# Kernel optimization log

Hardware: AMD Instinct MI355X
Metric: run time of the kernel (lower is better)

## Reference

```python
import jax, jax.numpy as jnp
import numpy as np

N, H, W, C, CK, ITER = 4, 256, 256, 8, 2, 4
HID = 2 * C
C2 = C * C


def project(x, w1, b1, w2, b2, w3, b3):
    # flax Project: Dense->gelu->Dense->gelu->Dense (gelu approximate=tanh, jax default)
    h = jax.nn.gelu(x @ w1 + b1)
    h = jax.nn.gelu(h @ w2 + b2)
    return h @ w3 + b3


def setup_inputs() -> dict:
    key = jax.random.key(0)
    ks = jax.random.split(key, 40)
    d = {}
    d['u'] = jax.random.normal(ks[0], (N, H, W, C), jnp.float32)
    d['k'] = jax.random.normal(ks[1], (N, H, W, CK), jnp.float32)
    idx = 2
    # gamma MLP (in CK), delta MLP (in CK), greens real/imag MLPs (in 2)
    for nm, fin in zip(['g', 'dl', 'fr', 'fi'], [CK, CK, 2, 2]):
        for li, (fi_, fo) in enumerate([(fin, HID), (HID, HID), (HID, C2)]):
            d[f'{nm}_w{li+1}'] = jax.random.normal(ks[idx], (fi_, fo), jnp.float32) / np.sqrt(fi_).astype(np.float32)
            d[f'{nm}_b{li+1}'] = jnp.zeros((fo,), jnp.float32)
            idx += 1
    d['bias'] = jax.random.normal(ks[idx], (C,), jnp.float32)
    return d


def reference(u, k, g_w1, g_b1, g_w2, g_b2, g_w3, g_b3,
              dl_w1, dl_b1, dl_w2, dl_b2, dl_w3, dl_b3,
              fr_w1, fr_b1, fr_w2, fr_b2, fr_w3, fr_b3,
              fi_w1, fi_b1, fi_w2, fi_b2, fi_w3, fi_b3, bias):
    # per-pixel gamma / delta matrices: (N,H,W,C,C), scaled by 1/C^2 as in original
    gmat = (project(k, g_w1, g_b1, g_w2, g_b2, g_w3, g_b3) / C2).reshape(N, H, W, C, C)
    dmat = (project(k, dl_w1, dl_b1, dl_w2, dl_b2, dl_w3, dl_b3) / C2).reshape(N, H, W, C, C)
    # spectral Green's filter on the rfft grid; meshgrid(kx, ky) -> (W, H//2+1)
    kx = jnp.fft.rfftfreq(H, d=1.0 / H)
    ky = jnp.fft.fftfreq(W, d=1.0 / W)
    Kx, Ky = jnp.meshgrid(kx, ky)
    K = jnp.stack([Kx, Ky], axis=-1).astype(jnp.float32)  # (W, H//2+1, 2)
    filt_r = project(K, fr_w1, fr_b1, fr_w2, fr_b2, fr_w3, fr_b3)
    filt_i = project(K, fi_w1, fi_b1, fi_w2, fi_b2, fi_w3, fi_b3)
    filt = ((filt_r + 1j * filt_i) / C2).reshape(W, H // 2 + 1, C, C)  # H==W
    for _ in range(ITER):
        local = 2.0 * u - jnp.einsum('nhwj,nhwjk->nhwk', u, gmat)
        du = jnp.einsum('nhwj,nhwjk->nhwk', u, dmat)
        uf = jnp.fft.rfftn(du, axes=(1, 2))  # (N,H,W//2+1,C) complex
        gu = jnp.fft.irfftn(jnp.einsum('nhwj,hwjk->nhwk', uf, filt), axes=(1, 2))
        u = local + jnp.einsum('nhwj,nhwjk->nhwk', gu, gmat)
    return jax.nn.gelu(u + bias)
```

## Files before the change

kernel.cpp:

```cpp
#include <hip/hip_runtime.h>
#include <math.h>

#define NB 4
#define HB 256
#define WB 256
#define CB 8
#define NPIX (NB*HB*WB)
#define W2B 129
#define TWO_PI_F 6.283185307179586f

typedef float f32x4 __attribute__((ext_vector_type(4)));

__device__ __forceinline__ float gelu_f(float x){
    float z = 0.7978845608028654f*(x + 0.044715f*x*x*x);
    return x * __builtin_amdgcn_rcpf(1.0f + __expf(-2.0f*z));
}

__device__ __forceinline__ unsigned pack_bf16x2(float a, float b){
    unsigned ua = __float_as_uint(a), ub = __float_as_uint(b);
    ua = (ua + 0x7FFFu + ((ua >> 16) & 1u)) >> 16;
    ub = (ub + 0x7FFFu + ((ub >> 16) & 1u)) >> 16;
    return ua | (ub << 16);
}
__device__ __forceinline__ float2 unpack_bf16x2(unsigned v){
    return make_float2(__uint_as_float(v << 16), __uint_as_float(v & 0xFFFF0000u));
}

__device__ __forceinline__ void ldcp(float* dst, const float* __restrict__ src, int n, int t){
    for (int i = t; i < n; i += 256) dst[i] = src[i];
}

__global__ __launch_bounds__(256) void prep_kernel(
    const float* __restrict__ kin,
    const float* gw1,const float* gb1,const float* gw2,const float* gb2,const float* gw3,const float* gb3,
    const float* dw1,const float* db1,const float* dw2,const float* db2,const float* dw3,const float* db3,
    const float* fw1,const float* fb1,const float* fw2,const float* fb2,const float* fw3,const float* fb3,
    const float* iw1,const float* ib1,const float* iw2,const float* ib2,const float* iw3,const float* ib3,
    unsigned* __restrict__ gmat, unsigned* __restrict__ dmat,
    unsigned* __restrict__ fpack)
{
    __shared__ __align__(16) float sw[2816];
    int t = threadIdx.x;
    int b = blockIdx.x;
    if (b >= 129){
        int gd = (b >= 641);
        const float* w1 = gd ? dw1 : gw1;  const float* b1 = gd ? db1 : gb1;
        const float* w2 = gd ? dw2 : gw2;  const float* b2 = gd ? db2 : gb2;
        const float* w3 = gd ? dw3 : gw3;  const float* b3 = gd ? db3 : gb3;
        ldcp(sw+0,   w1,  32, t); ldcp(sw+32,  b1, 16, t);
        ldcp(sw+48,  w2, 256, t); ldcp(sw+304, b2, 16, t);
        ldcp(sw+320, w3,1024, t); ldcp(sw+1344,b3, 64, t);
        __syncthreads();
        unsigned* mat = gd ? dmat : gmat;
        int p0 = (b - (gd ? 641 : 129))*512 + t;
        int p1 = p0 + 256;
        float2 kv0 = ((const float2*)kin)[p0];
        float2 kv1 = ((const float2*)kin)[p1];
        size_t base0 = (size_t)(p0 >> 6)*2048 + (size_t)(p0 & 63)*4;
        size_t base1 = (size_t)(p1 >> 6)*2048 + (size_t)(p1 & 63)*4;
        float h1[2][16], h2[2][16];
#pragma unroll
        for (int o = 0; o < 16; ++o){
            float wx = sw[o], wy = sw[16+o], bo = sw[32+o];
            h1[0][o] = gelu_f(kv0.x*wx + kv0.y*wy + bo);
            h1[1][o] = gelu_f(kv1.x*wx + kv1.y*wy + bo);
        }
#pragma unroll
        for (int oc = 0; oc < 4; ++oc){
            f32x4 bb = *(const f32x4*)(sw + 304 + oc*4);
            f32x4 a0 = bb, a1 = bb;
#pragma unroll
            for (int i = 0; i < 16; ++i){
                f32x4 w = *(const f32x4*)(sw + 48 + i*16 + oc*4);
                a0 += h1[0][i]*w; a1 += h1[1][i]*w;
            }
            h2[0][oc*4+0]=gelu_f(a0.x); h2[0][oc*4+1]=gelu_f(a0.y);
            h2[0][oc*4+2]=gelu_f(a0.z); h2[0][oc*4+3]=gelu_f(a0.w);
            h2[1][oc*4+0]=gelu_f(a1.x); h2[1][oc*4+1]=gelu_f(a1.y);
            h2[1][oc*4+2]=gelu_f(a1.z); h2[1][oc*4+3]=gelu_f(a1.w);
        }
        const float s = 1.0f/64.0f;
#pragma unroll
        for (int j = 0; j < 8; ++j){
            f32x4 bA = *(const f32x4*)(sw + 1344 + j*8);
            f32x4 bB = *(const f32x4*)(sw + 1344 + j*8 + 4);
            f32x4 A0 = bA, A1 = bB, B0 = bA, B1 = bB;
#pragma unroll
            for (int i = 0; i < 16; ++i){
                f32x4 wA = *(const f32x4*)(sw + 320 + i*64 + j*8);
                f32x4 wB = *(const f32x4*)(sw + 320 + i*64 + j*8 + 4);
                float h0 = h2[0][i], h1v = h2[1][i];
                A0 += h0*wA; A1 += h0*wB;
                B0 += h1v*wA; B1 += h1v*wB;
            }
            uint4 o0 = { pack_bf16x2(A0.x*s,A0.y*s), pack_bf16x2(A0.z*s,A0.w*s),
                         pack_bf16x2(A1.x*s,A1.y*s), pack_bf16x2(A1.z*s,A1.w*s) };
            uint4 o1 = { pack_bf16x2(B0.x*s,B0.y*s), pack_bf16x2(B0.z*s,B0.w*s),
                         pack_bf16x2(B1.x*s,B1.y*s), pack_bf16x2(B1.z*s,B1.w*s) };
            *(uint4*)(mat + base0 + (size_t)j*256) = o0;
            *(uint4*)(mat + base1 + (size_t)j*256) = o1;
        }
    } else {
        ldcp(sw+0,   fw1,  32, t); ldcp(sw+32,  fb1, 16, t);
        ldcp(sw+48,  fw2, 256, t); ldcp(sw+304, fb2, 16, t);
        ldcp(sw+320, fw3,1024, t); ldcp(sw+1344,fb3, 64, t);
        ldcp(sw+1408+0,   iw1,  32, t); ldcp(sw+1408+32,  ib1, 16, t);
        ldcp(sw+1408+48,  iw2, 256, t); ldcp(sw+1408+304, ib2, 16, t);
        ldcp(sw+1408+320, iw3,1024, t); ldcp(sw+1408+1344,ib3, 64, t);
        __syncthreads();
        int w2 = b;
        float x = (float)w2;
        float y = (float)(t < 128 ? t : t - 256);
        float h1r[16], h1i[16], h2r[16], h2i[16];
#pragma unroll
        for (int o = 0; o < 16; ++o){
            h1r[o] = gelu_f(x*sw[o] + y*sw[16+o] + sw[32+o]);
            h1i[o] = gelu_f(x*sw[1408+o] + y*sw[1408+16+o] + sw[1408+32+o]);
        }
#pragma unroll
        for (int o = 0; o < 16; ++o){
            float ar = sw[304+o], ai = sw[1408+304+o];
#pragma unroll
            for (int i = 0; i < 16; ++i){
                ar += h1r[i]*sw[48+i*16+o];
                ai += h1i[i]*sw[1408+48+i*16+o];
            }
            h2r[o] = gelu_f(ar); h2i[o] = gelu_f(ai);
        }
        const float s = 1.0f/64.0f;
#pragma unroll
        for (int q = 0; q < 16; ++q){
            f32x4 aR = *(const f32x4*)(sw + 1344 + q*4);
            f32x4 aI = *(const f32x4*)(sw + 1408 + 1344 + q*4);
#pragma unroll
            for (int i = 0; i < 16; ++i){
                aR += h2r[i] * *(const f32x4*)(sw + 320 + i*64 + q*4);
                aI += h2i[i] * *(const f32x4*)(sw + 1408 + 320 + i*64 + q*4);
            }
            uint4 out = { pack_bf16x2(aR.x*s, aI.x*s), pack_bf16x2(aR.y*s, aI.y*s),
                          pack_bf16x2(aR.z*s, aI.z*s), pack_bf16x2(aR.w*s, aI.w*s) };
            *(uint4*)(fpack + (size_t)w2*16384 + (size_t)q*1024 + (size_t)t*4) = out;
        }
    }
}

__device__ __forceinline__ void fft256v(f32x4* xr, f32x4* xi, int t, float sgn)
{
    int n2 = t >> 4, k1 = t & 15;
    float csA, snA; __sincosf(sgn*TWO_PI_F*(float)k1*(1.0f/16.0f), &snA, &csA);
    f32x4 ar = {0.f,0.f,0.f,0.f}, ai = {0.f,0.f,0.f,0.f};
    float cw = 1.f, sw = 0.f;
#pragma unroll
    for (int n1 = 0; n1 < 16; ++n1){
        f32x4 vr = xr[16*n1 + n2], vi = xi[16*n1 + n2];
        ar += vr*cw - vi*sw;
        ai += vr*sw + vi*cw;
        float cn = cw*csA - sw*snA;
        sw = cw*snA + sw*csA; cw = cn;
    }
    float cs2, sn2; __sincosf(sgn*TWO_PI_F*(float)(n2*k1)*(1.0f/256.0f), &sn2, &cs2);
    f32x4 br = ar*cs2 - ai*sn2;
    f32x4 bi = ar*sn2 + ai*cs2;
    __syncthreads();
    xr[t] = br; xi[t] = bi;
    __syncthreads();
    int k1b = t & 15, k2 = t >> 4;
    float csB, snB; __sincosf(sgn*TWO_PI_F*(float)k2*(1.0f/16.0f), &snB, &csB);
    f32x4 yr = {0.f,0.f,0.f,0.f}, yi = {0.f,0.f,0.f,0.f};
    cw = 1.f; sw = 0.f;
#pragma unroll
    for (int n2b = 0; n2b < 16; ++n2b){
        f32x4 br2 = xr[n2b*16 + k1b], bi2 = xi[n2b*16 + k1b];
        yr += br2*cw - bi2*sw;
        yi += br2*sw + bi2*cw;
        float cn = cw*csB - sw*snB;
        sw = cw*snB + sw*csB; cw = cn;
    }
    __syncthreads();
    xr[t] = yr; xi[t] = yi;
    __syncthreads();
}

__device__ __forceinline__ void fft256v_core(f32x4* xr, f32x4* xi, int t, float sgn,
                                             f32x4& outR, f32x4& outI)
{
    int n2 = t >> 4, k1 = t & 15;
    float csA, snA; __sincosf(sgn*TWO_PI_F*(float)k1*(1.0f/16.0f), &snA, &csA);
    f32x4 ar = {0.f,0.f,0.f,0.f}, ai = {0.f,0.f,0.f,0.f};
    float cw = 1.f, sw = 0.f;
#pragma unroll
    for (int n1 = 0; n1 < 16; ++n1){
        f32x4 vr = xr[16*n1 + n2], vi = xi[16*n1 + n2];
        ar += vr*cw - vi*sw;
        ai += vr*sw + vi*cw;
        float cn = cw*csA - sw*snA;
        sw = cw*snA + sw*csA; cw = cn;
    }
    float cs2, sn2; __sincosf(sgn*TWO_PI_F*(float)(n2*k1)*(1.0f/256.0f), &sn2, &cs2);
    f32x4 br = ar*cs2 - ai*sn2;
    f32x4 bi = ar*sn2 + ai*cs2;
    __syncthreads();
    xr[t] = br; xi[t] = bi;
    __syncthreads();
    int k1b = t & 15, k2 = t >> 4;
    float csB, snB; __sincosf(sgn*TWO_PI_F*(float)k2*(1.0f/16.0f), &snB, &csB);
    f32x4 yr = {0.f,0.f,0.f,0.f}, yi = {0.f,0.f,0.f,0.f};
    cw = 1.f; sw = 0.f;
#pragma unroll
    for (int n2b = 0; n2b < 16; ++n2b){
        f32x4 br2 = xr[n2b*16 + k1b], bi2 = xi[n2b*16 + k1b];
        yr += br2*cw - bi2*sw;
        yi += br2*sw + bi2*cw;
        float cn = cw*csB - sw*snB;
        sw = cw*snB + sw*csB; cw = cn;
    }
    outR = yr; outI = yi;
}

__device__ __forceinline__ void fwd_store(
    f32x4* XR, f32x4* XI, const float* dv, int t, int n, int h,
    float2* __restrict__ spec)
{
    XR[t] = (f32x4){dv[0],dv[2],dv[4],dv[6]};
    XI[t] = (f32x4){dv[1],dv[3],dv[5],dv[7]};
    __syncthreads();
    fft256v(XR, XI, t, -1.f);
    if (t <= 128){
        int m = (256 - t) & 255;
        f32x4 zr = XR[t], zi = XI[t], yr = XR[m], yi = XI[m];
        float4* dst = (float4*)(spec + (((size_t)n*129 + t)*256 + h)*8);
        dst[0] = make_float4(0.5f*(zr.x+yr.x), 0.5f*(zi.x-yi.x), 0.5f*(zi.x+yi.x), 0.5f*(yr.x-zr.x));
        dst[1] = make_float4(0.5f*(zr.y+yr.y), 0.5f*(zi.y-yi.y), 0.5f*(zi.y+yi.y), 0.5f*(yr.y-zr.y));
        dst[2] = make_float4(0.5f*(zr.z+yr.z), 0.5f*(zi.z-yi.z), 0.5f*(zi.z+yi.z), 0.5f*(yr.z-zr.z));
        dst[3] = make_float4(0.5f*(zr.w+yr.w), 0.5f*(zi.w-yi.w), 0.5f*(zi.w+yi.w), 0.5f*(yr.w-zr.w));
    }
}

__device__ __forceinline__ void inv_fft_to_gu(
    const float2* __restrict__ spec, f32x4* XR, f32x4* XI,
    int t, int n, int h, float* gu)
{
    int w2 = (t <= 128) ? t : 256 - t;
    const float4* rp = (const float4*)(spec + (((size_t)n*129 + w2)*256 + h)*8);
    float4 q0 = rp[0], q1 = rp[1], q2 = rp[2], q3 = rp[3];
    f32x4 xr, xi;
    if (t <= 128){
        xr = (f32x4){q0.x - q0.w, q1.x - q1.w, q2.x - q2.w, q3.x - q3.w};
        xi = (f32x4){q0.y + q0.z, q1.y + q1.z, q2.y + q2.z, q3.y + q3.z};
    } else {
        xr = (f32x4){ q0.x + q0.w,  q1.x + q1.w,  q2.x + q2.w,  q3.x + q3.w};
        xi = (f32x4){-q0.y + q0.z, -q1.y + q1.z, -q2.y + q2.z, -q3.y + q3.z};
    }
    XR[t] = xr; XI[t] = xi;
    __syncthreads();
    f32x4 gr, gi;
    fft256v_core(XR, XI, t, +1.f, gr, gi);
    const float s = 1.0f/65536.0f;
    gu[0]=gr.x*s; gu[1]=gi.x*s; gu[2]=gr.y*s; gu[3]=gi.y*s;
    gu[4]=gr.z*s; gu[5]=gi.z*s; gu[6]=gr.w*s; gu[7]=gi.w*s;
}

__device__ __forceinline__ void matvec_acc(const unsigned* __restrict__ mat,
                                           size_t base, const float* v, float* acc)
{
    const uint4* mp = (const uint4*)(mat + base);
#pragma unroll
    for (int j = 0; j < 8; ++j){
        uint4 q = mp[j*64];
        float vj = v[j];
        float2 f0 = unpack_bf16x2(q.x), f1 = unpack_bf16x2(q.y);
        float2 f2 = unpack_bf16x2(q.z), f3 = unpack_bf16x2(q.w);
        acc[0] += vj*f0.x; acc[1] += vj*f0.y;
        acc[2] += vj*f1.x; acc[3] += vj*f1.y;
        acc[4] += vj*f2.x; acc[5] += vj*f2.y;
        acc[6] += vj*f3.x; acc[7] += vj*f3.y;
    }
}

__global__ __launch_bounds__(256) void fft_fwd_kernel(
    const float* __restrict__ u, const unsigned* __restrict__ dmat,
    float2* __restrict__ spec)
{
    __shared__ f32x4 XR[256], XI[256];
    int t = threadIdx.x, bid = blockIdx.x;
    int n = bid >> 8, h = bid & 255;
    const float* up = u + (size_t)bid*2048 + (size_t)t*8;
    float4 ua = ((const float4*)up)[0], ub = ((const float4*)up)[1];
    float uv[8] = {ua.x,ua.y,ua.z,ua.w, ub.x,ub.y,ub.z,ub.w};
    size_t base = (size_t)(bid*4 + (t>>6))*2048 + (size_t)(t&63)*4;
    float dv[8] = {0,0,0,0,0,0,0,0};
    matvec_acc(dmat, base, uv, dv);
    fwd_store(XR, XI, dv, t, n, h, spec);
}

__global__ __launch_bounds__(512) void ffth_mult_kernel(
    float2* __restrict__ spec, const unsigned* __restrict__ fpack)
{
    __shared__ f32x4 XR[2][256], XI[2][256];
    int tid = threadIdx.x;
    int t = tid & 255, g = tid >> 8;
    int n = blockIdx.x / 129, w2 = blockIdx.x % 129;
    float2* base = spec + ((size_t)(n*129 + w2))*2048;
    const float4* rp = (const float4*)(base + (size_t)t*8);
    float4 ra = rp[g*2], rb = rp[g*2+1];
    XR[g][t] = (f32x4){ra.x, ra.z, rb.x, rb.z};
    XI[g][t] = (f32x4){ra.y, ra.w, rb.y, rb.w};
    __syncthreads();
    f32x4 sR, sI;
    fft256v_core(XR[g], XI[g], t, -1.f, sR, sI);
    __syncthreads();
    XR[g][t] = sR; XI[g][t] = sI;
    __syncthreads();
    f32x4 oR = XR[1-g][t], oI = XI[1-g][t];
    f32x4 aR = g ? oR : sR, aI = g ? oI : sI;
    f32x4 bR = g ? sR : oR, bI = g ? sI : oI;
    float sr[8] = {aR.x,aR.y,aR.z,aR.w, bR.x,bR.y,bR.z,bR.w};
    float si[8] = {aI.x,aI.y,aI.z,aI.w, bI.x,bI.y,bI.z,bI.w};
    f32x4 orr = {0.f,0.f,0.f,0.f}, oii = {0.f,0.f,0.f,0.f};
    const uint4* fp = (const uint4*)(fpack + (size_t)w2*16384 + (size_t)t*4);
#pragma unroll
    for (int j = 0; j < 8; ++j){
        float sjr = sr[j], sji = si[j];
        uint4 fq = fp[(j*2 + g)*256];
        float2 f0 = unpack_bf16x2(fq.x), f1 = unpack_bf16x2(fq.y);
        float2 f2 = unpack_bf16x2(fq.z), f3 = unpack_bf16x2(fq.w);
        orr.x += sjr*f0.x - sji*f0.y;  oii.x += sjr*f0.y + sji*f0.x;
        orr.y += sjr*f1.x - sji*f1.y;  oii.y += sjr*f1.y + sji*f1.x;
        orr.z += sjr*f2.x - sji*f2.y;  oii.z += sjr*f2.y + sji*f2.x;
        orr.w += sjr*f3.x - sji*f3.y;  oii.w += sjr*f3.y + sji*f3.x;
    }
    __syncthreads();
    XR[g][t] = orr; XI[g][t] = oii;
    __syncthreads();
    f32x4 vR, vI;
    fft256v_core(XR[g], XI[g], t, +1.f, vR, vI);
    float4* wp = (float4*)(base + (size_t)t*8);
    wp[g*2]   = make_float4(vR.x, vI.x, vR.y, vI.y);
    wp[g*2+1] = make_float4(vR.z, vI.z, vR.w, vI.w);
}

__global__ __launch_bounds__(256) void born_step_kernel(
    float2* __restrict__ spec, const float* __restrict__ u_in,
    float* __restrict__ u_out, const unsigned* __restrict__ gmat,
    const unsigned* __restrict__ dmat)
{
    __shared__ f32x4 XR[256], XI[256];
    int t = threadIdx.x, bid = blockIdx.x;
    int n = bid >> 8, h = bid & 255;
    float gu[8];
    inv_fft_to_gu(spec, XR, XI, t, n, h, gu);

    const float* up = u_in + (size_t)bid*2048 + (size_t)t*8;
    float4 ua = ((const float4*)up)[0], ub = ((const float4*)up)[1];
    float uv[8] = {ua.x,ua.y,ua.z,ua.w, ub.x,ub.y,ub.z,ub.w};
    float e[8], acc[8];
#pragma unroll
    for (int c = 0; c < 8; ++c){ e[c] = gu[c] - uv[c]; acc[c] = 2.0f*uv[c]; }
    size_t base = (size_t)(bid*4 + (t>>6))*2048 + (size_t)(t&63)*4;
    matvec_acc(gmat, base, e, acc);
    float* op = u_out + (size_t)bid*2048 + (size_t)t*8;
    ((float4*)op)[0] = make_float4(acc[0],acc[1],acc[2],acc[3]);
    ((float4*)op)[1] = make_float4(acc[4],acc[5],acc[6],acc[7]);

    float dv[8] = {0,0,0,0,0,0,0,0};
    matvec_acc(dmat, base, acc, dv);
    __syncthreads();
    fwd_store(XR, XI, dv, t, n, h, spec);
}

__global__ __launch_bounds__(256) void final_kernel(
    const float2* __restrict__ spec, const float* __restrict__ u_in,
    const unsigned* __restrict__ gmat, const float* __restrict__ bias,
    float* __restrict__ out)
{
    __shared__ f32x4 XR[256], XI[256];
    int t = threadIdx.x, bid = blockIdx.x;
    int n = bid >> 8, h = bid & 255;
    float gu[8];
    inv_fft_to_gu(spec, XR, XI, t, n, h, gu);

    const float* up = u_in + (size_t)bid*2048 + (size_t)t*8;
    float4 ua = ((const float4*)up)[0], ub = ((const float4*)up)[1];
    float uv[8] = {ua.x,ua.y,ua.z,ua.w, ub.x,ub.y,ub.z,ub.w};
    float e[8], acc[8];
#pragma unroll
    for (int c = 0; c < 8; ++c){ e[c] = gu[c] - uv[c]; acc[c] = 2.0f*uv[c]; }
    size_t base = (size_t)(bid*4 + (t>>6))*2048 + (size_t)(t&63)*4;
    matvec_acc(gmat, base, e, acc);
#pragma unroll
    for (int k = 0; k < 8; ++k) acc[k] = gelu_f(acc[k] + bias[k]);
    float* op = out + (size_t)bid*2048 + (size_t)t*8;
    ((float4*)op)[0] = make_float4(acc[0],acc[1],acc[2],acc[3]);
    ((float4*)op)[1] = make_float4(acc[4],acc[5],acc[6],acc[7]);
}

extern "C" void kernel_launch(void* const* d_in, const int* in_sizes, int n_in,
                              void* d_out, int out_size, void* d_ws, size_t ws_size,
                              hipStream_t stream) {
    const float* u_in = (const float*)d_in[0];
    const float* k_in = (const float*)d_in[1];
    const float* Wp[24];
    for (int i = 0; i < 24; ++i) Wp[i] = (const float*)d_in[2+i];
    const float* bias = (const float*)d_in[26];

    char* base = (char*)d_ws;
    unsigned* gmat  = (unsigned*)(base);
    unsigned* dmat  = (unsigned*)(base + 33554432ull);
    unsigned* fpack = (unsigned*)(base + 67108864ull);
    float*    u_ws  = (float*)   (base + 75563008ull);
    float2*   spec  = (float2*)  (base + 83951616ull);

    prep_kernel<<<1153, 256, 0, stream>>>(k_in,
        Wp[0],Wp[1],Wp[2],Wp[3],Wp[4],Wp[5],
        Wp[6],Wp[7],Wp[8],Wp[9],Wp[10],Wp[11],
        Wp[12],Wp[13],Wp[14],Wp[15],Wp[16],Wp[17],
        Wp[18],Wp[19],Wp[20],Wp[21],Wp[22],Wp[23],
        gmat, dmat, fpack);

    fft_fwd_kernel<<<1024, 256, 0, stream>>>(u_in, dmat, spec);
    for (int it = 0; it < 4; ++it){
        ffth_mult_kernel<<<516, 512, 0, stream>>>(spec, fpack);
        if (it < 3){
            born_step_kernel<<<1024, 256, 0, stream>>>(
                spec, (it == 0) ? u_in : u_ws, u_ws, gmat, dmat);
        } else {
            final_kernel<<<1024, 256, 0, stream>>>(spec, u_ws, gmat, bias, (float*)d_out);
        }
    }
}
```

Measured before the change: 220.1 us.

## Restructure prep MLP: one pixel per thread for both matrices, LDS-staged final layer

Each block now loads both the gamma and delta MLP weights and computes the first two layers for one pixel per thread, writing the hidden activations into a padded shared buffer. For the 16->64 output layer, each thread takes one output row j and four pixels at a time, holding its weight slices in registers and reading the hidden values from shared memory. This replaces the old scheme of two pixels per thread with the full 64-wide output, and is meant to cut register pressure and redundant weight loads from LDS. In exchange it adds block barriers and LDS traffic for the hidden values, and it changes the write pattern to gmat/dmat.

New measurement: 227.9 us. +3.6%, slower.

```diff
diff --git a/kernel.cpp b/kernel.cpp
--- a/kernel.cpp
+++ b/kernel.cpp
@@ -40,65 +40,77 @@
     unsigned* __restrict__ fpack)
 {
     __shared__ __align__(16) float sw[2816];
+    __shared__ float hbuf[256*17];
     int t = threadIdx.x;
     int b = blockIdx.x;
     if (b >= 129){
-        int gd = (b >= 641);
-        const float* w1 = gd ? dw1 : gw1;  const float* b1 = gd ? db1 : gb1;
-        const float* w2 = gd ? dw2 : gw2;  const float* b2 = gd ? db2 : gb2;
-        const float* w3 = gd ? dw3 : gw3;  const float* b3 = gd ? db3 : gb3;
-        ldcp(sw+0,   w1,  32, t); ldcp(sw+32,  b1, 16, t);
-        ldcp(sw+48,  w2, 256, t); ldcp(sw+304, b2, 16, t);
-        ldcp(sw+320, w3,1024, t); ldcp(sw+1344,b3, 64, t);
+        ldcp(sw+0,   gw1,  32, t); ldcp(sw+32,  gb1, 16, t);
+        ldcp(sw+48,  gw2, 256, t); ldcp(sw+304, gb2, 16, t);
+        ldcp(sw+320, gw3,1024, t); ldcp(sw+1344,gb3, 64, t);
+        ldcp(sw+1408+0,   dw1,  32, t); ldcp(sw+1408+32,  db1, 16, t);
+        ldcp(sw+1408+48,  dw2, 256, t); ldcp(sw+1408+304, db2, 16, t);
+        ldcp(sw+1408+320, dw3,1024, t); ldcp(sw+1408+1344,db3, 64, t);
         __syncthreads();
-        unsigned* mat = gd ? dmat : gmat;
-        int p0 = (b - (gd ? 641 : 129))*512 + t;
-        int p1 = p0 + 256;
-        float2 kv0 = ((const float2*)kin)[p0];
-        float2 kv1 = ((const float2*)kin)[p1];
-        size_t base0 = (size_t)(p0 >> 6)*2048 + (size_t)(p0 & 63)*4;
-        size_t base1 = (size_t)(p1 >> 6)*2048 + (size_t)(p1 & 63)*4;
-        float h1[2][16], h2[2][16];
-#pragma unroll
-        for (int o = 0; o < 16; ++o){
-            float wx = sw[o], wy = sw[16+o], bo = sw[32+o];
-            h1[0][o] = gelu_f(kv0.x*wx + kv0.y*wy + bo);
-            h1[1][o] = gelu_f(kv1.x*wx + kv1.y*wy + bo);
-        }
-#pragma unroll
-        for (int oc = 0; oc < 4; ++oc){
-            f32x4 bb = *(const f32x4*)(sw + 304 + oc*4);
-            f32x4 a0 = bb, a1 = bb;
-#pragma unroll
-            for (int i = 0; i < 16; ++i){
-                f32x4 w = *(const f32x4*)(sw + 48 + i*16 + oc*4);
-                a0 += h1[0][i]*w; a1 += h1[1][i]*w;
+        int pix0 = (b - 129)*256;
+        float2 kv = ((const float2*)kin)[pix0 + t];
+        int j = t & 7, g = t >> 3;
+        const float s = 1.0f/64.0f;
+#pragma unroll
+        for (int m = 0; m < 2; ++m){
+            const float* W = sw + m*1408;
+            unsigned* mat = m ? dmat : gmat;
+            float h1[16];
+#pragma unroll
+            for (int o = 0; o < 16; ++o)
+                h1[o] = gelu_f(kv.x*W[o] + kv.y*W[16+o] + W[32+o]);
+#pragma unroll
+            for (int oc = 0; oc < 4; ++oc){
+                f32x4 acc = *(const f32x4*)(W + 304 + oc*4);
+#pragma unroll
+                for (int i = 0; i < 16; ++i)
+                    acc += h1[i] * *(const f32x4*)(W + 48 + i*16 + oc*4);
+                hbuf[t*17+oc*4+0] = gelu_f(acc.x);
+                hbuf[t*17+oc*4+1] = gelu_f(acc.y);
+                hbuf[t*17+oc*4+2] = gelu_f(acc.z);
+                hbuf[t*17+oc*4+3] = gelu_f(acc.w);
             }
-            h2[0][oc*4+0]=gelu_f(a0.x); h2[0][oc*4+1]=gelu_f(a0.y);
-            h2[0][oc*4+2]=gelu_f(a0.z); h2[0][oc*4+3]=gelu_f(a0.w);
-            h2[1][oc*4+0]=gelu_f(a1.x); h2[1][oc*4+1]=gelu_f(a1.y);
-            h2[1][oc*4+2]=gelu_f(a1.z); h2[1][oc*4+3]=gelu_f(a1.w);
-        }
-        const float s = 1.0f/64.0f;
-#pragma unroll
-        for (int j = 0; j < 8; ++j){
-            f32x4 bA = *(const f32x4*)(sw + 1344 + j*8);
-            f32x4 bB = *(const f32x4*)(sw + 1344 + j*8 + 4);
-            f32x4 A0 = bA, A1 = bB, B0 = bA, B1 = bB;
-#pragma unroll
-            for (int i = 0; i < 16; ++i){
-                f32x4 wA = *(const f32x4*)(sw + 320 + i*64 + j*8);
-                f32x4 wB = *(const f32x4*)(sw + 320 + i*64 + j*8 + 4);
-                float h0 = h2[0][i], h1v = h2[1][i];
-                A0 += h0*wA; A1 += h0*wB;
-                B0 += h1v*wA; B1 += h1v*wB;
+            __syncthreads();
+            f32x4 bA = *(const f32x4*)(W + 1344 + j*8);
+            f32x4 bB = *(const f32x4*)(W + 1344 + j*8 + 4);
+#pragma unroll
+            for (int pc = 0; pc < 2; ++pc){
+                f32x4 A0_0=bA, A1_0=bB, A0_1=bA, A1_1=bB;
+                f32x4 A0_2=bA, A1_2=bB, A0_3=bA, A1_3=bB;
+#pragma unroll
+                for (int ic = 0; ic < 2; ++ic){
+                    f32x4 wA[8], wB[8];
+#pragma unroll
+                    for (int i = 0; i < 8; ++i){
+                        wA[i] = *(const f32x4*)(W + 320 + (ic*8+i)*64 + j*8);
+                        wB[i] = *(const f32x4*)(W + 320 + (ic*8+i)*64 + j*8 + 4);
+                    }
+                    const float* hp = hbuf + (g*8 + pc*4)*17 + ic*8;
+#pragma unroll
+                    for (int i = 0; i < 8; ++i){
+                        float h0 = hp[i], h1v = hp[17+i], h2v = hp[34+i], h3v = hp[51+i];
+                        A0_0 += h0*wA[i];  A1_0 += h0*wB[i];
+                        A0_1 += h1v*wA[i]; A1_1 += h1v*wB[i];
+                        A0_2 += h2v*wA[i]; A1_2 += h2v*wB[i];
+                        A0_3 += h3v*wA[i]; A1_3 += h3v*wB[i];
+                    }
+                }
+                int pxl = g*8 + pc*4;
+#pragma unroll
+                for (int p = 0; p < 4; ++p){
+                    f32x4 A0 = p==0?A0_0 : p==1?A0_1 : p==2?A0_2 : A0_3;
+                    f32x4 A1 = p==0?A1_0 : p==1?A1_1 : p==2?A1_2 : A1_3;
+                    int pix = pix0 + pxl + p;
+                    uint4 o = { pack_bf16x2(A0.x*s,A0.y*s), pack_bf16x2(A0.z*s,A0.w*s),
+                                pack_bf16x2(A1.x*s,A1.y*s), pack_bf16x2(A1.z*s,A1.w*s) };
+                    *(uint4*)(mat + (size_t)(pix>>6)*2048 + (size_t)j*256 + (size_t)(pix&63)*4) = o;
+                }
             }
-            uint4 o0 = { pack_bf16x2(A0.x*s,A0.y*s), pack_bf16x2(A0.z*s,A0.w*s),
-                         pack_bf16x2(A1.x*s,A1.y*s), pack_bf16x2(A1.z*s,A1.w*s) };
-            uint4 o1 = { pack_bf16x2(B0.x*s,B0.y*s), pack_bf16x2(B0.z*s,B0.w*s),
-                         pack_bf16x2(B1.x*s,B1.y*s), pack_bf16x2(B1.z*s,B1.w*s) };
-            *(uint4*)(mat + base0 + (size_t)j*256) = o0;
-            *(uint4*)(mat + base1 + (size_t)j*256) = o1;
+            if (m == 0) __syncthreads();
         }
     } else {
         ldcp(sw+0,   fw1,  32, t); ldcp(sw+32,  fb1, 16, t);
```

## Process all 8 channels per thread in H-FFT multiply kernel with 256 threads

Applied to the files above, without the earlier changes.

The H-direction FFT + filter multiply kernel now uses 256 threads per block, each handling both 4-channel groups, where before it used 512 threads split into two groups. The exchange of FFT results between the two thread halves through shared memory is gone, along with one pair of barriers. Twiddle setup is now shared across twice the work. Each thread holds twice the registers, which may lower occupancy and latency hiding across the 516 blocks.

Result: faster. 211.0 us (-4.1%).

```diff
diff --git a/kernel.cpp b/kernel.cpp
--- a/kernel.cpp
+++ b/kernel.cpp
@@ -217,6 +217,47 @@
     outR = yr; outI = yi;
 }
 
+__device__ __forceinline__ void fft256v8_core(
+    f32x4 (*xr)[256], f32x4 (*xi)[256], int t, float sgn,
+    f32x4& o0R, f32x4& o0I, f32x4& o1R, f32x4& o1I)
+{
+    int n2 = t >> 4, k1 = t & 15;
+    float csA, snA; __sincosf(sgn*TWO_PI_F*(float)k1*(1.0f/16.0f), &snA, &csA);
+    f32x4 a0r={0.f,0.f,0.f,0.f}, a0i=a0r, a1r=a0r, a1i=a0r;
+    float cw = 1.f, sw = 0.f;
+#pragma unroll
+    for (int n1 = 0; n1 < 16; ++n1){
+        int idx = 16*n1 + n2;
+        f32x4 v0r = xr[0][idx], v0i = xi[0][idx];
+        f32x4 v1r = xr[1][idx], v1i = xi[1][idx];
+        a0r += v0r*cw - v0i*sw;  a0i += v0r*sw + v0i*cw;
+        a1r += v1r*cw - v1i*sw;  a1i += v1r*sw + v1i*cw;
+        float cn = cw*csA - sw*snA;
+        sw = cw*snA + sw*csA; cw = cn;
+    }
+    float cs2, sn2; __sincosf(sgn*TWO_PI_F*(float)(n2*k1)*(1.0f/256.0f), &sn2, &cs2);
+    f32x4 b0r = a0r*cs2 - a0i*sn2, b0i = a0r*sn2 + a0i*cs2;
+    f32x4 b1r = a1r*cs2 - a1i*sn2, b1i = a1r*sn2 + a1i*cs2;
+    __syncthreads();
+    xr[0][t]=b0r; xi[0][t]=b0i; xr[1][t]=b1r; xi[1][t]=b1i;
+    __syncthreads();
+    int k1b = t & 15, k2 = t >> 4;
+    float csB, snB; __sincosf(sgn*TWO_PI_F*(float)k2*(1.0f/16.0f), &snB, &csB);
+    f32x4 y0r={0.f,0.f,0.f,0.f}, y0i=y0r, y1r=y0r, y1i=y0r;
+    cw = 1.f; sw = 0.f;
+#pragma unroll
+    for (int n2b = 0; n2b < 16; ++n2b){
+        int idx = n2b*16 + k1b;
+        f32x4 c0r = xr[0][idx], c0i = xi[0][idx];
+        f32x4 c1r = xr[1][idx], c1i = xi[1][idx];
+        y0r += c0r*cw - c0i*sw;  y0i += c0r*sw + c0i*cw;
+        y1r += c1r*cw - c1i*sw;  y1i += c1r*sw + c1i*cw;
+        float cn = cw*csB - sw*snB;
+        sw = cw*snB + sw*csB; cw = cn;
+    }
+    o0R = y0r; o0I = y0i; o1R = y1r; o1I = y1i;
+}
+
 __device__ __forceinline__ void fwd_store(
     f32x4* XR, f32x4* XI, const float* dv, int t, int n, int h,
     float2* __restrict__ spec)
@@ -293,50 +334,55 @@
     fwd_store(XR, XI, dv, t, n, h, spec);
 }
 
-__global__ __launch_bounds__(512) void ffth_mult_kernel(
+__global__ __launch_bounds__(256) void ffth_mult_kernel(
     float2* __restrict__ spec, const unsigned* __restrict__ fpack)
 {
     __shared__ f32x4 XR[2][256], XI[2][256];
-    int tid = threadIdx.x;
-    int t = tid & 255, g = tid >> 8;
+    int t = threadIdx.x;
     int n = blockIdx.x / 129, w2 = blockIdx.x % 129;
     float2* base = spec + ((size_t)(n*129 + w2))*2048;
     const float4* rp = (const float4*)(base + (size_t)t*8);
-    float4 ra = rp[g*2], rb = rp[g*2+1];
-    XR[g][t] = (f32x4){ra.x, ra.z, rb.x, rb.z};
-    XI[g][t] = (f32x4){ra.y, ra.w, rb.y, rb.w};
-    __syncthreads();
-    f32x4 sR, sI;
-    fft256v_core(XR[g], XI[g], t, -1.f, sR, sI);
-    __syncthreads();
-    XR[g][t] = sR; XI[g][t] = sI;
-    __syncthreads();
-    f32x4 oR = XR[1-g][t], oI = XI[1-g][t];
-    f32x4 aR = g ? oR : sR, aI = g ? oI : sI;
-    f32x4 bR = g ? sR : oR, bI = g ? sI : oI;
-    float sr[8] = {aR.x,aR.y,aR.z,aR.w, bR.x,bR.y,bR.z,bR.w};
-    float si[8] = {aI.x,aI.y,aI.z,aI.w, bI.x,bI.y,bI.z,bI.w};
-    f32x4 orr = {0.f,0.f,0.f,0.f}, oii = {0.f,0.f,0.f,0.f};
+    float4 r0 = rp[0], r1 = rp[1], r2 = rp[2], r3 = rp[3];
+    XR[0][t] = (f32x4){r0.x, r0.z, r1.x, r1.z};
+    XI[0][t] = (f32x4){r0.y, r0.w, r1.y, r1.w};
+    XR[1][t] = (f32x4){r2.x, r2.z, r3.x, r3.z};
+    XI[1][t] = (f32x4){r2.y, r2.w, r3.y, r3.w};
+    __syncthreads();
+    f32x4 s0R, s0I, s1R, s1I;
+    fft256v8_core(XR, XI, t, -1.f, s0R, s0I, s1R, s1I);
+
+    float sr[8] = {s0R.x,s0R.y,s0R.z,s0R.w, s1R.x,s1R.y,s1R.z,s1R.w};
+    float si[8] = {s0I.x,s0I.y,s0I.z,s0I.w, s1I.x,s1I.y,s1I.z,s1I.w};
+    f32x4 o0R={0.f,0.f,0.f,0.f}, o0I=o0R, o1R=o0R, o1I=o0R;
     const uint4* fp = (const uint4*)(fpack + (size_t)w2*16384 + (size_t)t*4);
 #pragma unroll
     for (int j = 0; j < 8; ++j){
         float sjr = sr[j], sji = si[j];
-        uint4 fq = fp[(j*2 + g)*256];
-        float2 f0 = unpack_bf16x2(fq.x), f1 = unpack_bf16x2(fq.y);
-        float2 f2 = unpack_bf16x2(fq.z), f3 = unpack_bf16x2(fq.w);
-        orr.x += sjr*f0.x - sji*f0.y;  oii.x += sjr*f0.y + sji*f0.x;
-        orr.y += sjr*f1.x - sji*f1.y;  oii.y += sjr*f1.y + sji*f1.x;
-        orr.z += sjr*f2.x - sji*f2.y;  oii.z += sjr*f2.y + sji*f2.x;
-        orr.w += sjr*f3.x - sji*f3.y;  oii.w += sjr*f3.y + sji*f3.x;
-    }
-    __syncthreads();
-    XR[g][t] = orr; XI[g][t] = oii;
-    __syncthreads();
-    f32x4 vR, vI;
-    fft256v_core(XR[g], XI[g], t, +1.f, vR, vI);
+        uint4 fa = fp[(j*2+0)*256];
+        uint4 fb = fp[(j*2+1)*256];
+        float2 f0 = unpack_bf16x2(fa.x), f1 = unpack_bf16x2(fa.y);
+        float2 f2 = unpack_bf16x2(fa.z), f3 = unpack_bf16x2(fa.w);
+        o0R.x += sjr*f0.x - sji*f0.y;  o0I.x += sjr*f0.y + sji*f0.x;
+        o0R.y += sjr*f1.x - sji*f1.y;  o0I.y += sjr*f1.y + sji*f1.x;
+        o0R.z += sjr*f2.x - sji*f2.y;  o0I.z += sjr*f2.y + sji*f2.x;
+        o0R.w += sjr*f3.x - sji*f3.y;  o0I.w += sjr*f3.y + sji*f3.x;
+        float2 g0 = unpack_bf16x2(fb.x), g1 = unpack_bf16x2(fb.y);
+        float2 g2 = unpack_bf16x2(fb.z), g3 = unpack_bf16x2(fb.w);
+        o1R.x += sjr*g0.x - sji*g0.y;  o1I.x += sjr*g0.y + sji*g0.x;
+        o1R.y += sjr*g1.x - sji*g1.y;  o1I.y += sjr*g1.y + sji*g1.x;
+        o1R.z += sjr*g2.x - sji*g2.y;  o1I.z += sjr*g2.y + sji*g2.x;
+        o1R.w += sjr*g3.x - sji*g3.y;  o1I.w += sjr*g3.y + sji*g3.x;
+    }
+    __syncthreads();
+    XR[0][t]=o0R; XI[0][t]=o0I; XR[1][t]=o1R; XI[1][t]=o1I;
+    __syncthreads();
+    f32x4 v0R, v0I, v1R, v1I;
+    fft256v8_core(XR, XI, t, +1.f, v0R, v0I, v1R, v1I);
     float4* wp = (float4*)(base + (size_t)t*8);
-    wp[g*2]   = make_float4(vR.x, vI.x, vR.y, vI.y);
-    wp[g*2+1] = make_float4(vR.z, vI.z, vR.w, vI.w);
+    wp[0] = make_float4(v0R.x, v0I.x, v0R.y, v0I.y);
+    wp[1] = make_float4(v0R.z, v0I.z, v0R.w, v0I.w);
+    wp[2] = make_float4(v1R.x, v1I.x, v1R.y, v1I.y);
+    wp[3] = make_float4(v1R.z, v1I.z, v1R.w, v1I.w);
 }
 
 __global__ __launch_bounds__(256) void born_step_kernel(
@@ -419,7 +465,7 @@
 
     fft_fwd_kernel<<<1024, 256, 0, stream>>>(u_in, dmat, spec);
     for (int it = 0; it < 4; ++it){
-        ffth_mult_kernel<<<516, 512, 0, stream>>>(spec, fpack);
+        ffth_mult_kernel<<<516, 256, 0, stream>>>(spec, fpack);
         if (it < 3){
             born_step_kernel<<<1024, 256, 0, stream>>>(
                 spec, (it == 0) ? u_in : u_ws, u_ws, gmat, dmat);
```
